# Kernel optimization log

Hardware: AMD Instinct MI355X
Metric: run time of the kernel (lower is better)

The kernel has to match this reference:

```python
import math
from itertools import combinations
import jax, jax.numpy as jnp
import numpy as np

SEQ_LEN = 8
D_IN = 2048
D_OUT = 1152
TSS = 3          # temporal_set_size
WAY = 5
SHOT = 5
N_SUPPORT = WAY * SHOT
N_Q = 100
PE_SCALE = 0.1
LN_EPS = 1e-5

TUPLES = np.array(list(combinations(range(SEQ_LEN), TSS)), dtype=np.int32)  # [56, 3]
T_LEN = TUPLES.shape[0]  # 56


def _positional_encoding(seq_len, d):
    pos = np.arange(seq_len, dtype=np.float32)[:, None]
    div = np.exp(np.arange(0, d, 2, dtype=np.float32) * -(math.log(10000.0) / d))
    pe = np.zeros((seq_len, d), dtype=np.float32)
    pe[:, 0::2] = np.sin(pos * div) * PE_SCALE
    pe[:, 1::2] = np.cos(pos * div) * PE_SCALE
    return jnp.asarray(pe)


def _layernorm(x, g, b):
    mu = jnp.mean(x, axis=-1, keepdims=True)
    var = jnp.mean((x - mu) ** 2, axis=-1, keepdims=True)
    return (x - mu) * jax.lax.rsqrt(var + LN_EPS) * g + b


def setup_inputs() -> dict:
    key = jax.random.key(0)
    ks = jax.random.split(key, 6)
    support_set = jax.random.normal(ks[0], (N_SUPPORT, SEQ_LEN, D_IN), dtype=jnp.float32)
    queries = jax.random.normal(ks[1], (N_Q, SEQ_LEN, D_IN), dtype=jnp.float32)
    # sorted episode layout: class c occupies rows [c*SHOT, (c+1)*SHOT)
    support_labels = jnp.repeat(jnp.arange(WAY, dtype=jnp.int64), SHOT)
    d_flat = TSS * D_IN  # 6144
    k_w = jax.random.normal(ks[2], (d_flat, D_OUT), dtype=jnp.float32) * 0.02
    k_b = jnp.zeros((D_OUT,), dtype=jnp.float32)
    v_w = jax.random.normal(ks[3], (d_flat, D_OUT), dtype=jnp.float32) * 0.02
    v_b = jnp.zeros((D_OUT,), dtype=jnp.float32)
    ln_g = jnp.ones((D_OUT,), dtype=jnp.float32)
    ln_b = jnp.zeros((D_OUT,), dtype=jnp.float32)
    return {"support_set": support_set, "queries": queries,
            "support_labels": support_labels,
            "k_w": k_w, "k_b": k_b, "v_w": v_w, "v_b": v_b,
            "ln_g": ln_g, "ln_b": ln_b}


def reference(support_set, queries, support_labels, k_w, k_b, v_w, v_b, ln_g, ln_b):
    pe = _positional_encoding(SEQ_LEN, D_IN)  # dropout is identity in eval mode
    s = support_set + pe
    q = queries + pe

    def tuplify(x):  # [N, S, D] -> [N, T_LEN, TSS*D]
        return x[:, TUPLES, :].reshape(x.shape[0], T_LEN, TSS * D_IN)

    s_t = tuplify(s)
    q_t = tuplify(q)

    sk = _layernorm(s_t @ k_w + k_b, ln_g, ln_b)  # [25, 56, 1152]
    qk = _layernorm(q_t @ k_w + k_b, ln_g, ln_b)  # [100, 56, 1152]
    sv = s_t @ v_w + v_b                           # [25, 56, 1152]
    qv = q_t @ v_w + v_b                           # [100, 56, 1152]

    scale = 1.0 / math.sqrt(D_OUT)
    dists = []
    align = None
    for c in range(WAY):  # fixed small class loop; class rows are a static slice
        class_k = sk[c * SHOT:(c + 1) * SHOT]  # [SHOT, 56, 1152]
        class_v = sv[c * SHOT:(c + 1) * SHOT]
        # scores: [Q, T, K, T] == torch permute(0,2,1,3) of [Q, K, T, T]
        scores = jnp.einsum('qtd,ksd->qtks', qk, class_k) * scale
        flat = scores.reshape(N_Q, T_LEN, SHOT * T_LEN)
        sm = jax.nn.softmax(flat, axis=-1)
        sm = sm.reshape(N_Q, T_LEN, SHOT, T_LEN).transpose(0, 2, 1, 3)  # [Q, K, T, T]
        align = sm.sum(axis=1)  # [Q, T, T]
        proto = jnp.einsum('qkts,ksd->qtd', sm, class_v)  # [Q, 56, 1152]
        diff = qv - proto
        dists.append(-jnp.sum(diff * diff, axis=(-2, -1)) / T_LEN)  # [Q]
    logits = jnp.stack(dists, axis=1)  # [Q, WAY]
    return logits, align
```

## Files before the change

kernel.cpp:

```cpp
#include <hip/hip_runtime.h>
#include <hip/hip_bf16.h>
#include <math.h>

#define SEQ_LEN 8
#define D_IN 2048
#define D_OUT 1152
#define WAY 5
#define SHOT 5
#define N_SUPPORT 25
#define N_Q 100
#define N_SEQ 125
#define N_ROWS 1000
#define T_LEN 56
#define KS_LEN 280
#define KS_PAD 288
#define NCOLS 6912
#define MQT 5600
#define DPC 18

typedef __attribute__((ext_vector_type(4))) float f32x4;
typedef __attribute__((ext_vector_type(8))) short bf16x8;

__constant__ int TUP[T_LEN][3] = {
  {0,1,2},{0,1,3},{0,1,4},{0,1,5},{0,1,6},{0,1,7},{0,2,3},{0,2,4},{0,2,5},{0,2,6},
  {0,2,7},{0,3,4},{0,3,5},{0,3,6},{0,3,7},{0,4,5},{0,4,6},{0,4,7},{0,5,6},{0,5,7},
  {0,6,7},{1,2,3},{1,2,4},{1,2,5},{1,2,6},{1,2,7},{1,3,4},{1,3,5},{1,3,6},{1,3,7},
  {1,4,5},{1,4,6},{1,4,7},{1,5,6},{1,5,7},{1,6,7},{2,3,4},{2,3,5},{2,3,6},{2,3,7},
  {2,4,5},{2,4,6},{2,4,7},{2,5,6},{2,5,7},{2,6,7},{3,4,5},{3,4,6},{3,4,7},{3,5,6},
  {3,5,7},{3,6,7},{4,5,6},{4,5,7},{4,6,7},{5,6,7}
};

__device__ __forceinline__ ushort f2bf(float f) {
  union { float f; unsigned u; } v; v.f = f;
  unsigned r = v.u + 0x7FFFu + ((v.u >> 16) & 1u);
  return (ushort)(r >> 16);
}
__device__ __forceinline__ float bf2f(ushort u) {
  union { unsigned u; float f; } v; v.u = ((unsigned)u) << 16;
  return v.f;
}
__device__ __forceinline__ void gload16(const void* g, const void* l) {
  __builtin_amdgcn_global_load_lds(
      (const __attribute__((address_space(1))) unsigned int*)g,
      (__attribute__((address_space(3))) unsigned int*)l, 16, 0, 0);
}

__global__ __launch_bounds__(256) void pe_add(const float* __restrict__ sup,
                                              const float* __restrict__ que,
                                              ushort* __restrict__ X) {
  int idx = blockIdx.x * 256 + threadIdx.x;
  if (idx >= N_ROWS * D_IN) return;
  int d = idx & (D_IN - 1);
  int r = idx >> 11;
  int i = r & 7;
  int h2 = d & ~1;
  float freq = expf((float)h2 * (-9.210340371976184f / (float)D_IN));
  float ang = (float)i * freq;
  float pe = ((d & 1) ? cosf(ang) : sinf(ang)) * 0.1f;
  float src = (r < N_SUPPORT * SEQ_LEN) ? sup[idx] : que[idx - N_SUPPORT * SEQ_LEN * D_IN];
  X[idx] = f2bf(src + pe);
}

__global__ __launch_bounds__(256) void wtrans(const float* __restrict__ kw,
                                              const float* __restrict__ vw,
                                              ushort* __restrict__ WT) {
  __shared__ float tile[64][65];
  int bx = blockIdx.x;
  int by = blockIdx.y;
  int b = bx / 18;
  int n0 = (bx % 18) * 64;
  int k0 = by * 64;
  const float* src = ((b & 1) ? vw : kw) + (size_t)(b >> 1) * D_IN * D_OUT;
  int tid = threadIdx.x;
#pragma unroll
  for (int it = 0; it < 4; ++it) {
    int lin4 = it * 256 + tid;
    int kk = lin4 >> 4;
    int n4 = (lin4 & 15) * 4;
    float4 v = *(const float4*)(src + (size_t)(k0 + kk) * D_OUT + n0 + n4);
    tile[kk][n4 + 0] = v.x; tile[kk][n4 + 1] = v.y;
    tile[kk][n4 + 2] = v.z; tile[kk][n4 + 3] = v.w;
  }
  __syncthreads();
#pragma unroll
  for (int it = 0; it < 4; ++it) {
    int lin = it * 1024 + tid * 4;
    int nn = lin >> 6, kk = lin & 63;
    ushort4 o;
    o.x = f2bf(tile[kk + 0][nn]); o.y = f2bf(tile[kk + 1][nn]);
    o.z = f2bf(tile[kk + 2][nn]); o.w = f2bf(tile[kk + 3][nn]);
    *(ushort4*)&WT[((size_t)(b * D_OUT + n0 + nn)) * D_IN + k0 + kk] = o;
  }
}

template<int EPI, int NT>
__global__ __launch_bounds__(256) void gemm_bt(
    const ushort* __restrict__ A, const ushort* __restrict__ BT,
    float* __restrict__ C,
    const ushort* __restrict__ QV, float* __restrict__ DP,
    int M, int N, int K, int lda, int ldb, int ldc, float alpha,
    long batchA, long batchB, long batchC) {
  constexpr int JF = NT / 32;
  constexpr int NCHUNK = 8 + NT / 16;
  __shared__ ushort As[128][32];
  __shared__ ushort Bs[NT][32];
  int z = blockIdx.z;
  A  += (size_t)z * batchA;
  BT += (size_t)z * batchB;
  if constexpr (EPI < 2) C  += (size_t)z * batchC;
  else                   DP += (size_t)z * batchC;

  int tid = threadIdx.x;
  int wid = tid >> 6, lane = tid & 63;
  int l16 = lane & 15, lk = lane >> 4;
  int wr = wid >> 1, wc = wid & 1;
  int row0 = blockIdx.x * 128, col0 = blockIdx.y * NT;
  int lrow = lane >> 2, lcol = (lane & 3) * 8;

  f32x4 acc[4][JF] = {};
  for (int k0 = 0; k0 < K; k0 += 32) {
    for (int c = wid; c < NCHUNK; c += 4) {
      if (c < 8) {
        int grow = row0 + c * 16 + lrow;
        grow = grow < M ? grow : M - 1;
        gload16(A + (size_t)grow * lda + k0 + lcol, &As[c * 16][0]);
      } else {
        int gcol = col0 + (c - 8) * 16 + lrow;
        gcol = gcol < N ? gcol : N - 1;
        gload16(BT + (size_t)gcol * ldb + k0 + lcol, &Bs[(c - 8) * 16][0]);
      }
    }
    __syncthreads();
    bf16x8 af[4], bv[JF];
#pragma unroll
    for (int m = 0; m < 4; ++m) af[m] = *(const bf16x8*)&As[wr * 64 + m * 16 + l16][lk * 8];
#pragma unroll
    for (int j = 0; j < JF; ++j) bv[j] = *(const bf16x8*)&Bs[wc * (NT / 2) + j * 16 + l16][lk * 8];
#pragma unroll
    for (int m = 0; m < 4; ++m)
#pragma unroll
      for (int j = 0; j < JF; ++j)
        acc[m][j] = __builtin_amdgcn_mfma_f32_16x16x32_bf16(af[m], bv[j], acc[m][j], 0, 0, 0);
    __syncthreads();
  }

  if constexpr (EPI < 2) {
#pragma unroll
    for (int m = 0; m < 4; ++m)
#pragma unroll
      for (int j = 0; j < JF; ++j) {
        int col = col0 + wc * (NT / 2) + j * 16 + l16;
#pragma unroll
        for (int r = 0; r < 4; ++r) {
          int row = row0 + wr * 64 + m * 16 + lk * 4 + r;
          if (row < M && col < N)
            C[(size_t)row * ldc + col] = (EPI == 1) ? acc[m][j][r] * alpha : acc[m][j][r];
        }
      }
  } else {
    float sq[4][4] = {};
#pragma unroll
    for (int m = 0; m < 4; ++m)
#pragma unroll
      for (int j = 0; j < JF; ++j) {
        int col = col0 + wc * (NT / 2) + j * 16 + l16;
#pragma unroll
        for (int r = 0; r < 4; ++r) {
          int row = row0 + wr * 64 + m * 16 + lk * 4 + r;
          if (row < M) {
            float qvv = bf2f(QV[(size_t)row * D_OUT + col]);
            float d = qvv - acc[m][j][r];
            sq[m][r] += d * d;
          }
        }
      }
#pragma unroll
    for (int m = 0; m < 4; ++m)
#pragma unroll
      for (int r = 0; r < 4; ++r) {
        sq[m][r] += __shfl_xor(sq[m][r], 1);
        sq[m][r] += __shfl_xor(sq[m][r], 2);
        sq[m][r] += __shfl_xor(sq[m][r], 4);
        sq[m][r] += __shfl_xor(sq[m][r], 8);
      }
    if (l16 == 0) {
#pragma unroll
      for (int m = 0; m < 4; ++m)
#pragma unroll
        for (int r = 0; r < 4; ++r) {
          int row = row0 + wr * 64 + m * 16 + lk * 4 + r;
          if (row < M) DP[(size_t)row * DPC + blockIdx.y * 2 + wc] = sq[m][r];
        }
    }
  }
}

__global__ __launch_bounds__(256) void combine_ln(const float* __restrict__ G,
                                                  const float* __restrict__ kb,
                                                  const float* __restrict__ vb,
                                                  const float* __restrict__ lng,
                                                  const float* __restrict__ lnb,
                                                  ushort* __restrict__ skbf,
                                                  ushort* __restrict__ qkbf,
                                                  ushort* __restrict__ sv,
                                                  ushort* __restrict__ qvbf) {
  int t = blockIdx.x;
  int n = blockIdx.y;
  const float* g0 = G + (size_t)(n * 8 + TUP[t][0]) * NCOLS;
  const float* g1 = G + (size_t)(n * 8 + TUP[t][1]) * NCOLS + 2 * D_OUT;
  const float* g2 = G + (size_t)(n * 8 + TUP[t][2]) * NCOLS + 4 * D_OUT;
  __shared__ float kbuf[D_OUT];
  __shared__ float red1[256], red2[256];
  int tid = threadIdx.x;
  bool isq = (n >= N_SUPPORT);
  int c = n / SHOT, s = n % SHOT;
  ushort* vout = isq ? qvbf + ((size_t)(n - N_SUPPORT) * T_LEN + t) * D_OUT
                     : sv + ((size_t)c * KS_PAD + s * T_LEN + t) * D_OUT;
  float s1 = 0.f, s2 = 0.f;
  for (int d4 = tid; d4 < D_OUT / 4; d4 += 256) {
    int d = d4 * 4;
    float4 a = *(const float4*)(g0 + d);
    float4 b = *(const float4*)(g0 + D_OUT + d);
    float4 c1 = *(const float4*)(g1 + d);
    float4 c2 = *(const float4*)(g1 + D_OUT + d);
    float4 e1 = *(const float4*)(g2 + d);
    float4 e2 = *(const float4*)(g2 + D_OUT + d);
    float4 kb4 = *(const float4*)(kb + d);
    float4 vb4 = *(const float4*)(vb + d);
    float kx = a.x + c1.x + e1.x + kb4.x, ky = a.y + c1.y + e1.y + kb4.y;
    float kz = a.z + c1.z + e1.z + kb4.z, kw = a.w + c1.w + e1.w + kb4.w;
    float vx = b.x + c2.x + e2.x + vb4.x, vy = b.y + c2.y + e2.y + vb4.y;
    float vz = b.z + c2.z + e2.z + vb4.z, vw = b.w + c2.w + e2.w + vb4.w;
    *(float4*)(kbuf + d) = make_float4(kx, ky, kz, kw);
    ushort4 vv; vv.x = f2bf(vx); vv.y = f2bf(vy); vv.z = f2bf(vz); vv.w = f2bf(vw);
    *(ushort4*)(vout + d) = vv;
    s1 += kx + ky + kz + kw;
    s2 += kx * kx + ky * ky + kz * kz + kw * kw;
  }
  red1[tid] = s1; red2[tid] = s2;
  __syncthreads();
  for (int sft = 128; sft > 0; sft >>= 1) {
    if (tid < sft) { red1[tid] += red1[tid + sft]; red2[tid] += red2[tid + sft]; }
    __syncthreads();
  }
  float mu = red1[0] * (1.0f / D_OUT);
  float var = red2[0] * (1.0f / D_OUT) - mu * mu;
  float rs = rsqrtf(var + 1e-5f);
  ushort* kout = isq ? qkbf + ((size_t)(n - N_SUPPORT) * T_LEN + t) * D_OUT
                     : skbf + ((size_t)c * KS_PAD + s * T_LEN + t) * D_OUT;
  for (int d4 = tid; d4 < D_OUT / 4; d4 += 256) {
    int d = d4 * 4;
    float4 kv = *(const float4*)(kbuf + d);
    float4 g4 = *(const float4*)(lng + d);
    float4 b4 = *(const float4*)(lnb + d);
    ushort4 o;
    o.x = f2bf((kv.x - mu) * rs * g4.x + b4.x);
    o.y = f2bf((kv.y - mu) * rs * g4.y + b4.y);
    o.z = f2bf((kv.z - mu) * rs * g4.z + b4.z);
    o.w = f2bf((kv.w - mu) * rs * g4.w + b4.w);
    *(ushort4*)(kout + d) = o;
  }
}

__global__ __launch_bounds__(256) void svtrans(const ushort* __restrict__ sv,
                                               ushort* __restrict__ svT) {
  __shared__ ushort tile[32][65];
  int c = blockIdx.z;
  int d0 = blockIdx.x * 64;
  int k0 = blockIdx.y * 32;
  const ushort* src = sv + (size_t)c * KS_PAD * D_OUT;
  ushort* dst = svT + (size_t)c * D_OUT * KS_PAD;
  int tid = threadIdx.x;
#pragma unroll
  for (int it = 0; it < 8; ++it) {
    int lin = it * 256 + tid;
    int ks = k0 + (lin >> 6), d = d0 + (lin & 63);
    tile[lin >> 6][lin & 63] = (ks < KS_LEN) ? src[(size_t)ks * D_OUT + d] : (ushort)0;
  }
  __syncthreads();
#pragma unroll
  for (int it = 0; it < 8; ++it) {
    int lin = it * 256 + tid;
    int d = lin >> 5, ks = lin & 31;
    dst[(size_t)(d0 + d) * KS_PAD + k0 + ks] = tile[ks][d];
  }
}

__global__ __launch_bounds__(256) void softmax_align(const float* __restrict__ S,
                                                     ushort* __restrict__ sm,
                                                     float* __restrict__ align_out) {
  __shared__ float pl[4][KS_LEN];
  int wid = threadIdx.x >> 6, lane = threadIdx.x & 63;
  int row = blockIdx.x * 4 + wid;
  const float* src = S + (size_t)row * KS_PAD;
  float v[5];
  float mx = -1e30f;
#pragma unroll
  for (int j = 0; j < 5; ++j) {
    int ks = lane + j * 64;
    v[j] = (ks < KS_LEN) ? src[ks] : -1e30f;
    mx = fmaxf(mx, v[j]);
  }
#pragma unroll
  for (int m = 32; m > 0; m >>= 1) mx = fmaxf(mx, __shfl_xor(mx, m));
  float sum = 0.f;
  float p[5];
#pragma unroll
  for (int j = 0; j < 5; ++j) {
    int ks = lane + j * 64;
    p[j] = (ks < KS_LEN) ? expf(v[j] - mx) : 0.f;
    sum += p[j];
  }
#pragma unroll
  for (int m = 32; m > 0; m >>= 1) sum += __shfl_xor(sum, m);
  float inv = 1.0f / sum;
  ushort* dst = sm + (size_t)row * KS_PAD;
#pragma unroll
  for (int j = 0; j < 5; ++j) {
    int ks = lane + j * 64;
    if (ks < KS_PAD) dst[ks] = f2bf((ks < KS_LEN) ? p[j] * inv : 0.f);
  }
  int c = row / MQT;
  if (c == WAY - 1) {
#pragma unroll
    for (int j = 0; j < 5; ++j) {
      int ks = lane + j * 64;
      if (ks < KS_LEN) pl[wid][ks] = p[j] * inv;
    }
    __syncthreads();
    if (lane < T_LEN) {
      float a = 0.f;
#pragma unroll
      for (int k = 0; k < SHOT; ++k) a += pl[wid][k * T_LEN + lane];
      int qt = row - (WAY - 1) * MQT;
      align_out[(size_t)(qt / T_LEN) * (T_LEN * T_LEN) + (qt % T_LEN) * T_LEN + lane] = a;
    }
  }
}

__global__ __launch_bounds__(256) void logits_k(const float* __restrict__ DP,
                                                float* __restrict__ out) {
  __shared__ float red[256];
  int q = blockIdx.x / WAY, c = blockIdx.x % WAY;
  const float* base = DP + ((size_t)c * MQT + q * T_LEN) * DPC;
  int tid = threadIdx.x;
  float s = 0.f;
  for (int i = tid; i < T_LEN * DPC; i += 256) s += base[i];
  red[tid] = s;
  __syncthreads();
  for (int sft = 128; sft > 0; sft >>= 1) {
    if (tid < sft) red[tid] += red[tid + sft];
    __syncthreads();
  }
  if (tid == 0) out[blockIdx.x] = -red[0] * (1.0f / T_LEN);
}

extern "C" void kernel_launch(void* const* d_in, const int* in_sizes, int n_in,
                              void* d_out, int out_size, void* d_ws, size_t ws_size,
                              hipStream_t stream) {
  const float* sup  = (const float*)d_in[0];
  const float* que  = (const float*)d_in[1];
  const float* k_w  = (const float*)d_in[3];
  const float* k_b  = (const float*)d_in[4];
  const float* v_w  = (const float*)d_in[5];
  const float* v_b  = (const float*)d_in[6];
  const float* ln_g = (const float*)d_in[7];
  const float* ln_b = (const float*)d_in[8];
  float* out = (float*)d_out;

  char* w = (char*)d_ws;
  ushort* Xbf  = (ushort*)(w + 0);
  ushort* WT   = (ushort*)(w + 4096000);
  float*  G    = (float*)(w + 32407552);
  ushort* sv   = (ushort*)(w + 0);
  float*  S    = (float*)(w + 0);
  ushort* smbf = (ushort*)(w + 32407552);
  float*  DP   = (float*)(w + 0);
  ushort* qkbf = (ushort*)(w + 60055552);
  ushort* skbf = (ushort*)(w + 72957952);
  ushort* svT  = (ushort*)(w + 76275712);
  ushort* qvbf = (ushort*)(w + 79593472);

  const float scale = 0.02946278254943948f;

  pe_add<<<dim3(8000), 256, 0, stream>>>(sup, que, Xbf);
  wtrans<<<dim3(108, 32), 256, 0, stream>>>(k_w, v_w, WT);
  gemm_bt<0, 64><<<dim3(8, 108, 1), 256, 0, stream>>>(
      Xbf, WT, G, nullptr, nullptr,
      N_ROWS, NCOLS, D_IN, D_IN, D_IN, NCOLS, 1.0f, 0, 0, 0);
  combine_ln<<<dim3(T_LEN, N_SEQ), 256, 0, stream>>>(
      G, k_b, v_b, ln_g, ln_b, skbf, qkbf, sv, qvbf);
  svtrans<<<dim3(18, 9, WAY), 256, 0, stream>>>(sv, svT);
  gemm_bt<1, 96><<<dim3(44, 3, WAY), 256, 0, stream>>>(
      qkbf, skbf, S, nullptr, nullptr,
      MQT, KS_PAD, D_OUT, D_OUT, D_OUT, KS_PAD, scale,
      0, (long)KS_PAD * D_OUT, (long)MQT * KS_PAD);
  softmax_align<<<dim3(7000), 256, 0, stream>>>(S, smbf, out + N_Q * WAY);
  gemm_bt<2, 128><<<dim3(44, 9, WAY), 256, 0, stream>>>(
      smbf, svT, nullptr, qvbf, DP,
      MQT, D_OUT, KS_PAD, KS_PAD, KS_PAD, 0, 1.0f,
      (long)MQT * KS_PAD, (long)D_OUT * KS_PAD, (long)MQT * DPC);
  logits_k<<<dim3(N_Q * WAY), 256, 0, stream>>>(DP, out);
}
```

Measured before the change: 237.6 us.

## Double-buffer GEMM LDS tiles with async prefetch and XOR-swizzled layout

Converts the bf16 MFMA GEMM main loop to a two-stage pipeline. It issues global-to-LDS loads for the next K tile before computing the current one, and waits with explicit vmcnt counts instead of full syncthreads. It also XOR-swizzles the 16-byte column slot within each LDS row to reduce bank conflicts on fragment reads. This doubles the LDS footprint, which may lower occupancy. It also relies on hand-computed per-wave vmcnt counts being correct.

```diff
diff --git a/kernel.cpp b/kernel.cpp
--- a/kernel.cpp
+++ b/kernel.cpp
@@ -44,6 +44,9 @@
       (const __attribute__((address_space(1))) unsigned int*)g,
       (__attribute__((address_space(3))) unsigned int*)l, 16, 0, 0);
 }
+template<int N> __device__ __forceinline__ void vmw() {
+  asm volatile("s_waitcnt vmcnt(%0)" :: "n"(N) : "memory");
+}
 
 __global__ __launch_bounds__(256) void pe_add(const float* __restrict__ sup,
                                               const float* __restrict__ que,
@@ -101,9 +104,9 @@
     int M, int N, int K, int lda, int ldb, int ldc, float alpha,
     long batchA, long batchB, long batchC) {
   constexpr int JF = NT / 32;
-  constexpr int NCHUNK = 8 + NT / 16;
-  __shared__ ushort As[128][32];
-  __shared__ ushort Bs[NT][32];
+  constexpr int NCH = 8 + NT / 16;
+  __shared__ ushort As[2][128][32];
+  __shared__ ushort Bs[2][NT][32];
   int z = blockIdx.z;
   A  += (size_t)z * batchA;
   BT += (size_t)z * batchB;
@@ -115,33 +118,56 @@
   int l16 = lane & 15, lk = lane >> 4;
   int wr = wid >> 1, wc = wid & 1;
   int row0 = blockIdx.x * 128, col0 = blockIdx.y * NT;
-  int lrow = lane >> 2, lcol = (lane & 3) * 8;
-
-  f32x4 acc[4][JF] = {};
-  for (int k0 = 0; k0 < K; k0 += 32) {
-    for (int c = wid; c < NCHUNK; c += 4) {
+  int lrow = lane >> 2;
+  int lcol = ((lane & 3) ^ ((lane >> 3) & 3)) * 8;
+  int rslot = (lk ^ ((l16 >> 1) & 3)) * 8;
+
+  auto stage = [&](int buf, int t) {
+    int k0 = t * 32;
+    for (int c = wid; c < NCH; c += 4) {
       if (c < 8) {
         int grow = row0 + c * 16 + lrow;
         grow = grow < M ? grow : M - 1;
-        gload16(A + (size_t)grow * lda + k0 + lcol, &As[c * 16][0]);
+        gload16(A + (size_t)grow * lda + k0 + lcol, &As[buf][c * 16][0]);
       } else {
         int gcol = col0 + (c - 8) * 16 + lrow;
         gcol = gcol < N ? gcol : N - 1;
-        gload16(BT + (size_t)gcol * ldb + k0 + lcol, &Bs[(c - 8) * 16][0]);
+        gload16(BT + (size_t)gcol * ldb + k0 + lcol, &Bs[buf][(c - 8) * 16][0]);
       }
     }
-    __syncthreads();
+  };
+
+  f32x4 acc[4][JF] = {};
+  int nk = K / 32;
+  stage(0, 0);
+  for (int t = 0; t < nk; ++t) {
+    int cur = t & 1;
+    if (t + 1 < nk) {
+      stage(cur ^ 1, t + 1);
+      if constexpr ((NCH & 3) == 0) {
+        vmw<NCH / 4>();
+      } else {
+        if (wid < (NCH & 3)) vmw<NCH / 4 + 1>(); else vmw<NCH / 4>();
+      }
+    } else {
+      vmw<0>();
+    }
+    __builtin_amdgcn_s_barrier();
+    __builtin_amdgcn_sched_barrier(0);
     bf16x8 af[4], bv[JF];
 #pragma unroll
-    for (int m = 0; m < 4; ++m) af[m] = *(const bf16x8*)&As[wr * 64 + m * 16 + l16][lk * 8];
-#pragma unroll
-    for (int j = 0; j < JF; ++j) bv[j] = *(const bf16x8*)&Bs[wc * (NT / 2) + j * 16 + l16][lk * 8];
+    for (int m = 0; m < 4; ++m)
+      af[m] = *(const bf16x8*)&As[cur][wr * 64 + m * 16 + l16][rslot];
+#pragma unroll
+    for (int j = 0; j < JF; ++j)
+      bv[j] = *(const bf16x8*)&Bs[cur][wc * (NT / 2) + j * 16 + l16][rslot];
 #pragma unroll
     for (int m = 0; m < 4; ++m)
 #pragma unroll
       for (int j = 0; j < JF; ++j)
         acc[m][j] = __builtin_amdgcn_mfma_f32_16x16x32_bf16(af[m], bv[j], acc[m][j], 0, 0, 0);
-    __syncthreads();
+    __builtin_amdgcn_sched_barrier(0);
+    __builtin_amdgcn_s_barrier();
   }
 
   if constexpr (EPI < 2) {
```

Measured after the change: 233.6 us. No clear change (-1.7%).
